# Optimization experiments

Hardware: AMD Instinct MI355X
Metric: run time of the kernel (lower is better)

## Reference

```python
import jax, jax.numpy as jnp
import numpy as np

B, T, E, H, VIN, VOUT = 64, 64, 64, 128, 256, 32000


def setup_inputs() -> dict:
    key = jax.random.key(0)
    ks = jax.random.split(key, 14)
    s = 0.08  # ~1/sqrt(hidden), torch-style init scale, avoids gate saturation
    return {
        "src": jax.random.randint(ks[0], (B, T), 0, VIN),
        "tgt": jax.random.randint(ks[1], (B, T), 0, VOUT),
        "enc_emb": jax.random.normal(ks[2], (VIN, E), jnp.float32) * s,
        "dec_emb": jax.random.normal(ks[3], (VOUT, E), jnp.float32) * s,
        "enc_Wih": jax.random.normal(ks[4], (4 * H, E), jnp.float32) * s,
        "enc_Whh": jax.random.normal(ks[5], (4 * H, H), jnp.float32) * s,
        "enc_bih": jax.random.normal(ks[6], (4 * H,), jnp.float32) * s,
        "enc_bhh": jax.random.normal(ks[7], (4 * H,), jnp.float32) * s,
        "dec_Wih": jax.random.normal(ks[8], (4 * H, E), jnp.float32) * s,
        "dec_Whh": jax.random.normal(ks[9], (4 * H, H), jnp.float32) * s,
        "dec_bih": jax.random.normal(ks[10], (4 * H,), jnp.float32) * s,
        "dec_bhh": jax.random.normal(ks[11], (4 * H,), jnp.float32) * s,
        "fc_W": jax.random.normal(ks[12], (VOUT, H), jnp.float32) * s,
        "fc_b": jax.random.normal(ks[13], (VOUT,), jnp.float32) * s,
    }


def _lstm(xs, h0, c0, Wih, Whh, bih, bhh):
    # xs: [T, B, E]; torch gate order i, f, g, o
    xg = jnp.einsum('tbe,ge->tbg', xs, Wih) + bih  # precompute input gates for all steps

    def step(carry, xg_t):
        h, c = carry
        gates = xg_t + h @ Whh.T + bhh  # [B, 4H]
        i, f, g, o = jnp.split(gates, 4, axis=-1)
        c = jax.nn.sigmoid(f) * c + jax.nn.sigmoid(i) * jnp.tanh(g)
        h = jax.nn.sigmoid(o) * jnp.tanh(c)
        return (h, c), h

    (h, c), hs = jax.lax.scan(step, (h0, c0), xg)
    return h, c, hs


def reference(src, tgt, enc_emb, dec_emb, enc_Wih, enc_Whh, enc_bih, enc_bhh,
              dec_Wih, dec_Whh, dec_bih, dec_bhh, fc_W, fc_b):
    # padding_idx=0: row 0 of embeddings is zero
    enc_emb = enc_emb.at[0].set(0.0)
    dec_emb = dec_emb.at[0].set(0.0)

    zeros = jnp.zeros((src.shape[0], H), jnp.float32)
    # encoder over full src
    x_src = enc_emb[src].transpose(1, 0, 2)  # [T, B, E]
    h, c, _ = _lstm(x_src, zeros, zeros, enc_Wih, enc_Whh, enc_bih, enc_bhh)
    # decoder with full teacher forcing: inputs are tgt[:, :-1]
    x_dec = dec_emb[tgt[:, :-1]].transpose(1, 0, 2)  # [T-1, B, E]
    _, _, hs = _lstm(x_dec, h, c, dec_Wih, dec_Whh, dec_bih, dec_bhh)
    logits = jnp.einsum('tbh,vh->tbv', hs, fc_W) + fc_b  # [T-1, B, V]
    out = jnp.concatenate(
        [jnp.zeros((1,) + logits.shape[1:], logits.dtype), logits], axis=0)
    return out.transpose(1, 0, 2)  # [B, T, V]; outputs[:, 0] == 0 as in torch
```

## Files before the change

### kernel.cpp

```cpp
#include <hip/hip_runtime.h>
#include <hip/hip_bf16.h>
#include <stddef.h>

#define BB 64
#define TTOT 64
#define EE 64
#define HH 128
#define G4 512
#define VIN 256
#define VOUT 32000

typedef __attribute__((ext_vector_type(8))) short bf16x8;
typedef __attribute__((ext_vector_type(4))) float f32x4;
typedef __attribute__((ext_vector_type(2))) float f32x2;

__device__ __forceinline__ unsigned short f2bf(float x) {
    unsigned int u = __float_as_uint(x);
    unsigned int r = (u + 0x7fffu + ((u >> 16) & 1u)) >> 16;
    return (unsigned short)r;
}

__device__ __forceinline__ float fsig(float x) {
    return 1.f / (1.f + __expf(-x));
}
__device__ __forceinline__ float ftanh(float x) {
    return 1.f - 2.f / (__expf(2.f * x) + 1.f);
}

__device__ __forceinline__ f32x2 pkfma(f32x2 a, f32x2 b, f32x2 d) {
    asm("v_pk_fma_f32 %0, %1, %2, %0" : "+v"(d) : "v"(a), "v"(b));
    return d;
}

__device__ __forceinline__ float quad_sum(float v) {
    v += __int_as_float(__builtin_amdgcn_mov_dpp(__float_as_int(v), 0xB1, 0xF, 0xF, true));
    v += __int_as_float(__builtin_amdgcn_mov_dpp(__float_as_int(v), 0x4E, 0xF, 0xF, true));
    return v;
}

__device__ __forceinline__ int hidx(int u) { return u + (u >> 5) * 8; }
#define HPAD 152

__global__ __launch_bounds__(512) void prep_k(const float* __restrict__ enc_emb,
                                              const float* __restrict__ eWih,
                                              const float* __restrict__ ebih,
                                              float* __restrict__ table,
                                              const int* __restrict__ tgt,
                                              const float* __restrict__ dec_emb,
                                              const float* __restrict__ dWih,
                                              const float* __restrict__ dbih,
                                              float* __restrict__ xg) {
    __shared__ __align__(16) float x[16][EE];
    int g = threadIdx.x;
    if (blockIdx.x < 256) {
        int v = blockIdx.x;
        if (g < EE) x[0][g] = (v == 0) ? 0.f : enc_emb[(size_t)v * EE + g];
        __syncthreads();
        float acc = ebih[g];
        const float* wr = eWih + (size_t)g * EE;
#pragma unroll
        for (int e = 0; e < EE; e += 4) {
            float4 w4 = *(const float4*)(wr + e);
            float4 x4 = *(const float4*)(&x[0][e]);
            acc = fmaf(x4.x, w4.x, acc);
            acc = fmaf(x4.y, w4.y, acc);
            acc = fmaf(x4.z, w4.z, acc);
            acc = fmaf(x4.w, w4.w, acc);
        }
        table[(size_t)v * G4 + g] = acc;
    } else {
        int p0 = (blockIdx.x - 256) * 16;
        {
            int e = g & 63;
#pragma unroll
            for (int half = 0; half < 2; ++half) {
                int pr = (g >> 6) + half * 8;
                int pair = p0 + pr;
                int t = pair >> 6, b = pair & 63;
                int tok = tgt[b * TTOT + t];
                x[pr][e] = (tok == 0) ? 0.f : dec_emb[(size_t)tok * EE + e];
            }
        }
        __syncthreads();
        float bi = dbih[g];
        float acc[16];
#pragma unroll
        for (int pr = 0; pr < 16; ++pr) acc[pr] = bi;
        const float* wr = dWih + (size_t)g * EE;
#pragma unroll
        for (int e = 0; e < EE; e += 4) {
            float4 w4 = *(const float4*)(wr + e);
#pragma unroll
            for (int pr = 0; pr < 16; ++pr) {
                float4 x4 = *(const float4*)(&x[pr][e]);
                acc[pr] = fmaf(x4.x, w4.x, acc[pr]);
                acc[pr] = fmaf(x4.y, w4.y, acc[pr]);
                acc[pr] = fmaf(x4.z, w4.z, acc[pr]);
                acc[pr] = fmaf(x4.w, w4.w, acc[pr]);
            }
        }
#pragma unroll
        for (int pr = 0; pr < 16; ++pr)
            xg[(size_t)(p0 + pr) * G4 + g] = acc[pr];
    }
}

__global__ __launch_bounds__(512) void lstm_k(const float* __restrict__ table,
                                              const int* __restrict__ src,
                                              const float* __restrict__ eWhh,
                                              const float* __restrict__ ebhh,
                                              const float* __restrict__ xg,
                                              const float* __restrict__ dWhh,
                                              const float* __restrict__ dbhh,
                                              unsigned short* __restrict__ hs,
                                              const float* __restrict__ fcW,
                                              unsigned short* __restrict__ fwb) {
    if (blockIdx.x >= BB) {
        int i0 = (blockIdx.x - BB) * 512 + threadIdx.x;
        const int n4 = VOUT * HH / 4;
        const int stride = 512 * 512;
#pragma unroll 1
        for (int i = i0; i < n4; i += stride) {
            float4 v = *(const float4*)(fcW + (size_t)i * 4);
            ushort4 o;
            o.x = f2bf(v.x); o.y = f2bf(v.y); o.z = f2bf(v.z); o.w = f2bf(v.w);
            *(ushort4*)(fwb + (size_t)i * 4) = o;
        }
        return;
    }

    int b = blockIdx.x;
    int tid = threadIdx.x;
    int u = tid >> 2, p = tid & 3;
    __shared__ __align__(16) float hbuf[2][HPAD];
    __shared__ int toks[TTOT];

    f32x2 w2[4][16];
#pragma unroll
    for (int q = 0; q < 4; ++q) {
        const float* wr = eWhh + (size_t)(q * HH + u) * HH + p * 32;
#pragma unroll
        for (int kk = 0; kk < 32; kk += 4) {
            float4 t4 = *(const float4*)(wr + kk);
            w2[q][kk >> 1] = (f32x2){t4.x, t4.y};
            w2[q][(kk >> 1) + 1] = (f32x2){t4.z, t4.w};
        }
    }
    if (tid < TTOT) toks[tid] = src[b * TTOT + tid];
    if (p == 0) {
        hbuf[0][hidx(u)] = 0.f;
        hs[((size_t)b << 13) + u] = 0;
    }
    float bb = ebhh[p * HH + u];
    float c = 0.f;
    __syncthreads();

    float xv = table[(size_t)toks[0] * G4 + p * HH + u];

#pragma unroll 1
    for (int t = 0; t < TTOT; ++t) {
        float xn = (t + 1 < TTOT) ? table[(size_t)toks[t + 1] * G4 + p * HH + u] : 0.f;
        const float* hq = &hbuf[t & 1][p * 40];
        float4 h4[8];
#pragma unroll
        for (int j = 0; j < 8; ++j) h4[j] = *(const float4*)(hq + j * 4);

        f32x2 a0 = (f32x2){0.f, 0.f}, a1 = a0, a2 = a0, a3 = a0;
#pragma unroll
        for (int j = 0; j < 8; ++j) {
            float4 h = h4[j];
            f32x2 hlo = (f32x2){h.x, h.y};
            f32x2 hhi = (f32x2){h.z, h.w};
            a0 = pkfma(hlo, w2[0][2 * j], a0); a0 = pkfma(hhi, w2[0][2 * j + 1], a0);
            a1 = pkfma(hlo, w2[1][2 * j], a1); a1 = pkfma(hhi, w2[1][2 * j + 1], a1);
            a2 = pkfma(hlo, w2[2][2 * j], a2); a2 = pkfma(hhi, w2[2][2 * j + 1], a2);
            a3 = pkfma(hlo, w2[3][2 * j], a3); a3 = pkfma(hhi, w2[3][2 * j + 1], a3);
        }
        float xb = xv + bb;
        float v0 = a0[0] + a0[1] + (p == 0 ? xb : 0.f);
        float v1 = a1[0] + a1[1] + (p == 1 ? xb : 0.f);
        float v2 = a2[0] + a2[1] + (p == 2 ? xb : 0.f);
        float v3 = a3[0] + a3[1] + (p == 3 ? xb : 0.f);
        v0 = quad_sum(v0); v1 = quad_sum(v1); v2 = quad_sum(v2); v3 = quad_sum(v3);

        float fi = fsig(v0), ff = fsig(v1), fg = ftanh(v2), fo = fsig(v3);
        c = ff * c + fi * fg;
        float hn = fo * ftanh(c);
        if (p == 0) hbuf[(t + 1) & 1][hidx(u)] = hn;
        __syncthreads();
        xv = xn;
    }

#pragma unroll
    for (int q = 0; q < 4; ++q) {
        const float* wr = dWhh + (size_t)(q * HH + u) * HH + p * 32;
#pragma unroll
        for (int kk = 0; kk < 32; kk += 4) {
            float4 t4 = *(const float4*)(wr + kk);
            w2[q][kk >> 1] = (f32x2){t4.x, t4.y};
            w2[q][(kk >> 1) + 1] = (f32x2){t4.z, t4.w};
        }
    }
    bb = dbhh[p * HH + u];
    float xv2 = xg[(size_t)b * G4 + p * HH + u];

#pragma unroll 1
    for (int t = 0; t < TTOT - 1; ++t) {
        float xn = (t + 1 < TTOT - 1) ? xg[((size_t)(t + 1) * BB + b) * G4 + p * HH + u] : 0.f;
        const float* hq = &hbuf[t & 1][p * 40];
        float4 h4[8];
#pragma unroll
        for (int j = 0; j < 8; ++j) h4[j] = *(const float4*)(hq + j * 4);

        f32x2 a0 = (f32x2){0.f, 0.f}, a1 = a0, a2 = a0, a3 = a0;
#pragma unroll
        for (int j = 0; j < 8; ++j) {
            float4 h = h4[j];
            f32x2 hlo = (f32x2){h.x, h.y};
            f32x2 hhi = (f32x2){h.z, h.w};
            a0 = pkfma(hlo, w2[0][2 * j], a0); a0 = pkfma(hhi, w2[0][2 * j + 1], a0);
            a1 = pkfma(hlo, w2[1][2 * j], a1); a1 = pkfma(hhi, w2[1][2 * j + 1], a1);
            a2 = pkfma(hlo, w2[2][2 * j], a2); a2 = pkfma(hhi, w2[2][2 * j + 1], a2);
            a3 = pkfma(hlo, w2[3][2 * j], a3); a3 = pkfma(hhi, w2[3][2 * j + 1], a3);
        }
        float xb = xv2 + bb;
        float v0 = a0[0] + a0[1] + (p == 0 ? xb : 0.f);
        float v1 = a1[0] + a1[1] + (p == 1 ? xb : 0.f);
        float v2 = a2[0] + a2[1] + (p == 2 ? xb : 0.f);
        float v3 = a3[0] + a3[1] + (p == 3 ? xb : 0.f);
        v0 = quad_sum(v0); v1 = quad_sum(v1); v2 = quad_sum(v2); v3 = quad_sum(v3);

        float fi = fsig(v0), ff = fsig(v1), fg = ftanh(v2), fo = fsig(v3);
        c = ff * c + fi * fg;
        float hn = fo * ftanh(c);
        if (p == 0) {
            hbuf[(t + 1) & 1][hidx(u)] = hn;
            hs[((size_t)b << 13) + ((size_t)(t + 1) << 7) + u] = f2bf(hn);
        }
        __syncthreads();
        xv2 = xn;
    }
}

#define LDSW 260
__global__ __launch_bounds__(256) void fc_k(const unsigned short* __restrict__ hs,
                                            const unsigned short* __restrict__ fw,
                                            const float* __restrict__ fb,
                                            float* __restrict__ out) {
    int id = blockIdx.x;
    int bq = id / 125;
    int nb = id % 125;
    int n0 = nb * 256;
    int wave = threadIdx.x >> 6;
    int lane = threadIdx.x & 63;
    int l15 = lane & 15;
    int kg = lane >> 4;

    __shared__ __align__(16) float lds[64 * LDSW];

    bf16x8 a[4][4];
#pragma unroll
    for (int i = 0; i < 4; ++i) {
        const unsigned short* arow = fw + (size_t)(n0 + (wave * 4 + i) * 16 + l15) * HH + kg * 8;
#pragma unroll
        for (int kt = 0; kt < 4; ++kt) a[i][kt] = *(const bf16x8*)(arow + kt * 32);
    }

    float4 biasv = *(const float4*)(fb + n0 + lane * 4);

#pragma unroll 1
    for (int bi = 0; bi < 16; ++bi) {
        int b = bq * 16 + bi;

        const unsigned short* ph = hs + ((size_t)b << 13);
        bf16x8 bfr[4][4];
#pragma unroll
        for (int ts = 0; ts < 4; ++ts) {
            const unsigned short* pr = ph + ((size_t)(ts * 16 + l15) << 7) + kg * 8;
#pragma unroll
            for (int kt = 0; kt < 4; ++kt) bfr[ts][kt] = *(const bf16x8*)(pr + kt * 32);
        }

#pragma unroll
        for (int i = 0; i < 4; ++i) {
            f32x4 ac0 = (f32x4){0.f, 0.f, 0.f, 0.f};
            f32x4 ac1 = (f32x4){0.f, 0.f, 0.f, 0.f};
            f32x4 ac2 = (f32x4){0.f, 0.f, 0.f, 0.f};
            f32x4 ac3 = (f32x4){0.f, 0.f, 0.f, 0.f};
#pragma unroll
            for (int kt = 0; kt < 4; ++kt) {
                ac0 = __builtin_amdgcn_mfma_f32_16x16x32_bf16(a[i][kt], bfr[0][kt], ac0, 0, 0, 0);
                ac1 = __builtin_amdgcn_mfma_f32_16x16x32_bf16(a[i][kt], bfr[1][kt], ac1, 0, 0, 0);
                ac2 = __builtin_amdgcn_mfma_f32_16x16x32_bf16(a[i][kt], bfr[2][kt], ac2, 0, 0, 0);
                ac3 = __builtin_amdgcn_mfma_f32_16x16x32_bf16(a[i][kt], bfr[3][kt], ac3, 0, 0, 0);
            }
            int nc = (wave * 4 + i) * 16 + kg * 4;
#define DUMP(ts, accv)                                                         \
            *(f32x4*)(&lds[(ts * 16 + l15) * LDSW + nc]) = accv;
            DUMP(0, ac0) DUMP(1, ac1) DUMP(2, ac2) DUMP(3, ac3)
#undef DUMP
        }
        __syncthreads();

        size_t outb = (size_t)b * TTOT * VOUT + n0 + lane * 4;
#pragma unroll
        for (int r = 0; r < 16; ++r) {
            int ot = wave * 16 + r;
            f32x4 v;
            if (ot == 0) {
                v = (f32x4){0.f, 0.f, 0.f, 0.f};
            } else {
                f32x4 s = *(const f32x4*)(&lds[ot * LDSW + lane * 4]);
                v[0] = s[0] + biasv.x; v[1] = s[1] + biasv.y;
                v[2] = s[2] + biasv.z; v[3] = s[3] + biasv.w;
            }
            *(f32x4*)(out + outb + (size_t)ot * VOUT) = v;
        }
        __syncthreads();
    }
}

extern "C" void kernel_launch(void* const* d_in, const int* in_sizes, int n_in,
                              void* d_out, int out_size, void* d_ws, size_t ws_size,
                              hipStream_t stream) {
    const int* src = (const int*)d_in[0];
    const int* tgt = (const int*)d_in[1];
    const float* enc_emb = (const float*)d_in[2];
    const float* dec_emb = (const float*)d_in[3];
    const float* enc_Wih = (const float*)d_in[4];
    const float* enc_Whh = (const float*)d_in[5];
    const float* enc_bih = (const float*)d_in[6];
    const float* enc_bhh = (const float*)d_in[7];
    const float* dec_Wih = (const float*)d_in[8];
    const float* dec_Whh = (const float*)d_in[9];
    const float* dec_bih = (const float*)d_in[10];
    const float* dec_bhh = (const float*)d_in[11];
    const float* fc_W = (const float*)d_in[12];
    const float* fc_b = (const float*)d_in[13];
    float* out = (float*)d_out;
    char* ws = (char*)d_ws;

    float* table = (float*)(ws + 0);
    unsigned short* hs = (unsigned short*)(ws + 524288);
    unsigned short* fwb = (unsigned short*)(ws + 1572864);
    float* xgd = (float*)(ws + 9764864);

    prep_k<<<256 + 252, 512, 0, stream>>>(enc_emb, enc_Wih, enc_bih, table,
                                          tgt, dec_emb, dec_Wih, dec_bih, xgd);
    lstm_k<<<BB + 512, 512, 0, stream>>>(table, src, enc_Whh, enc_bhh, xgd,
                                         dec_Whh, dec_bhh, hs, fc_W, fwb);
    fc_k<<<4 * 125, 256, 0, stream>>>(hs, fwb, fc_b, out);
}
```

Before: 253.2 us.

## Double-buffer FC output tile through LDS and use nontemporal stores

Splits each batch's 64-timestep tile into two 32-row halves and double-buffers the LDS staging area. The next half's gather and MFMA compute now overlap with storing the current half, and the loop needs one barrier per phase instead of two. Output stores become nontemporal to avoid polluting cache with the large logits tensor. This adds more phases and loop overhead, and register pressure may rise from the interleaving.

Result: faster. 241.1 us (median of 2 runs) (-4.8%).

```diff
diff --git a/kernel.cpp b/kernel.cpp
--- a/kernel.cpp
+++ b/kernel.cpp
@@ -242,7 +242,7 @@
     }
 }
 
-#define LDSW 260
+#define LDSW2 260
 __global__ __launch_bounds__(256) void fc_k(const unsigned short* __restrict__ hs,
                                             const unsigned short* __restrict__ fw,
                                             const float* __restrict__ fb,
@@ -256,7 +256,7 @@
     int l15 = lane & 15;
     int kg = lane >> 4;
 
-    __shared__ __align__(16) float lds[64 * LDSW];
+    __shared__ __align__(16) float lds[2][32 * LDSW2];
 
     bf16x8 a[4][4];
 #pragma unroll
@@ -265,59 +265,79 @@
 #pragma unroll
         for (int kt = 0; kt < 4; ++kt) a[i][kt] = *(const bf16x8*)(arow + kt * 32);
     }
-
     float4 biasv = *(const float4*)(fb + n0 + lane * 4);
 
+    bf16x8 bfr[2][4];
+
+#define GATHER(bv, hv)                                                            \
+    {                                                                             \
+        const unsigned short* ph_ = hs + ((size_t)(bv) << 13);                    \
+        _Pragma("unroll")                                                         \
+        for (int ts2 = 0; ts2 < 2; ++ts2) {                                       \
+            const unsigned short* pr_ =                                           \
+                ph_ + ((size_t)((hv) * 32 + ts2 * 16 + l15) << 7) + kg * 8;       \
+            _Pragma("unroll")                                                     \
+            for (int kt = 0; kt < 4; ++kt) bfr[ts2][kt] = *(const bf16x8*)(pr_ + kt * 32); \
+        }                                                                         \
+    }
+
+#define COMPUTE_DUMP(bufv)                                                        \
+    {                                                                             \
+        _Pragma("unroll")                                                         \
+        for (int i = 0; i < 4; ++i) {                                             \
+            _Pragma("unroll")                                                     \
+            for (int ts2 = 0; ts2 < 2; ++ts2) {                                   \
+                f32x4 acc = (f32x4){0.f, 0.f, 0.f, 0.f};                          \
+                _Pragma("unroll")                                                 \
+                for (int kt = 0; kt < 4; ++kt)                                    \
+                    acc = __builtin_amdgcn_mfma_f32_16x16x32_bf16(a[i][kt], bfr[ts2][kt], acc, 0, 0, 0); \
+                *(f32x4*)(&lds[bufv][(ts2 * 16 + l15) * LDSW2 + (wave * 4 + i) * 16 + kg * 4]) = acc; \
+            }                                                                     \
+        }                                                                         \
+    }
+
+#define STORE(bv, hv, bufv)                                                       \
+    {                                                                             \
+        size_t outb_ = (size_t)(bv) * TTOT * VOUT + n0 + lane * 4;                \
+        _Pragma("unroll")                                                         \
+        for (int r = 0; r < 8; ++r) {                                             \
+            int rloc = wave * 8 + r;                                              \
+            int ot = (hv) * 32 + rloc;                                            \
+            f32x4 v;                                                              \
+            if (ot == 0) {                                                        \
+                v = (f32x4){0.f, 0.f, 0.f, 0.f};                                  \
+            } else {                                                              \
+                f32x4 s = *(const f32x4*)(&lds[bufv][rloc * LDSW2 + lane * 4]);   \
+                v[0] = s[0] + biasv.x; v[1] = s[1] + biasv.y;                     \
+                v[2] = s[2] + biasv.z; v[3] = s[3] + biasv.w;                     \
+            }                                                                     \
+            __builtin_nontemporal_store(v, (f32x4*)(out + outb_ + (size_t)ot * VOUT)); \
+        }                                                                         \
+    }
+
+    GATHER(bq * 16, 0);
+    COMPUTE_DUMP(0);
+    __syncthreads();
+
 #pragma unroll 1
-    for (int bi = 0; bi < 16; ++bi) {
-        int b = bq * 16 + bi;
-
-        const unsigned short* ph = hs + ((size_t)b << 13);
-        bf16x8 bfr[4][4];
-#pragma unroll
-        for (int ts = 0; ts < 4; ++ts) {
-            const unsigned short* pr = ph + ((size_t)(ts * 16 + l15) << 7) + kg * 8;
-#pragma unroll
-            for (int kt = 0; kt < 4; ++kt) bfr[ts][kt] = *(const bf16x8*)(pr + kt * 32);
-        }
-
-#pragma unroll
-        for (int i = 0; i < 4; ++i) {
-            f32x4 ac0 = (f32x4){0.f, 0.f, 0.f, 0.f};
-            f32x4 ac1 = (f32x4){0.f, 0.f, 0.f, 0.f};
-            f32x4 ac2 = (f32x4){0.f, 0.f, 0.f, 0.f};
-            f32x4 ac3 = (f32x4){0.f, 0.f, 0.f, 0.f};
-#pragma unroll
-            for (int kt = 0; kt < 4; ++kt) {
-                ac0 = __builtin_amdgcn_mfma_f32_16x16x32_bf16(a[i][kt], bfr[0][kt], ac0, 0, 0, 0);
-                ac1 = __builtin_amdgcn_mfma_f32_16x16x32_bf16(a[i][kt], bfr[1][kt], ac1, 0, 0, 0);
-                ac2 = __builtin_amdgcn_mfma_f32_16x16x32_bf16(a[i][kt], bfr[2][kt], ac2, 0, 0, 0);
-                ac3 = __builtin_amdgcn_mfma_f32_16x16x32_bf16(a[i][kt], bfr[3][kt], ac3, 0, 0, 0);
-            }
-            int nc = (wave * 4 + i) * 16 + kg * 4;
-#define DUMP(ts, accv)                                                         \
-            *(f32x4*)(&lds[(ts * 16 + l15) * LDSW + nc]) = accv;
-            DUMP(0, ac0) DUMP(1, ac1) DUMP(2, ac2) DUMP(3, ac3)
-#undef DUMP
-        }
-        __syncthreads();
-
-        size_t outb = (size_t)b * TTOT * VOUT + n0 + lane * 4;
-#pragma unroll
-        for (int r = 0; r < 16; ++r) {
-            int ot = wave * 16 + r;
-            f32x4 v;
-            if (ot == 0) {
-                v = (f32x4){0.f, 0.f, 0.f, 0.f};
-            } else {
-                f32x4 s = *(const f32x4*)(&lds[ot * LDSW + lane * 4]);
-                v[0] = s[0] + biasv.x; v[1] = s[1] + biasv.y;
-                v[2] = s[2] + biasv.z; v[3] = s[3] + biasv.w;
-            }
-            *(f32x4*)(out + outb + (size_t)ot * VOUT) = v;
-        }
-        __syncthreads();
-    }
+    for (int ph = 0; ph < 32; ++ph) {
+        int cb = bq * 16 + (ph >> 1);
+        int chf = ph & 1;
+        int nph = ph + 1;
+        if (nph < 32) {
+            int nbv = bq * 16 + (nph >> 1);
+            int nhf = nph & 1;
+            GATHER(nbv, nhf);
+            STORE(cb, chf, ph & 1);
+            COMPUTE_DUMP(nph & 1);
+        } else {
+            STORE(cb, chf, ph & 1);
+        }
+        __syncthreads();
+    }
+#undef GATHER
+#undef COMPUTE_DUMP
+#undef STORE
 }
 
 extern "C" void kernel_launch(void* const* d_in, const int* in_sizes, int n_in,
```
